# Kernel optimization log

Measured on AMD Instinct MI355X. Metric: run time of the kernel, lower is better.

Reference implementation:

```python
import jax, jax.numpy as jnp
import numpy as np

OUT = 7        # RoIPool output_size
STRIDE = 16    # feature map stride (forward does cat_rois[:,1:] *= 1/16)


def setup_inputs() -> dict:
    key = jax.random.key(0)
    k1, k2, k3 = jax.random.split(key, 3)
    B, C, H, W, N = 2, 256, 50, 50, 128
    features = jax.random.normal(k1, (B, C, H, W), jnp.float32)
    im = jax.random.randint(k2, (N,), 0, B).astype(jnp.float32)
    # image-space coords in [0, 16*(H-1)] so rounded feature coords stay in-bounds
    coords = jax.random.uniform(k3, (N, 4), jnp.float32, 0.0, float(STRIDE * (H - 1)))
    x1 = jnp.minimum(coords[:, 0], coords[:, 2])
    x2 = jnp.maximum(coords[:, 0], coords[:, 2])
    y1 = jnp.minimum(coords[:, 1], coords[:, 3])
    y2 = jnp.maximum(coords[:, 1], coords[:, 3])
    cat_rois = jnp.stack([im, x1, y1, x2, y2], axis=1)
    return {"features": features, "cat_rois": cat_rois}


def _roi_pool(features, cat_rois):
    # cat_rois[:,1:] *= 1/16 ; round ; cast to int (as in the torch module)
    rois = cat_rois.at[:, 1:].multiply(1.0 / STRIDE)
    rois = jnp.round(rois).astype(jnp.int32)
    im = rois[:, 0]
    x1, y1, x2, y2 = rois[:, 1], rois[:, 2], rois[:, 3], rois[:, 4]
    h = y2 - y1 + 1  # slice y1:y2+1 -> height
    w = x2 - x1 + 1
    H, W = features.shape[2], features.shape[3]

    i = jnp.arange(OUT)
    # AdaptiveMaxPool2d bin boundaries: start=floor(i*h/OUT), end=ceil((i+1)*h/OUT)
    ys = (i[None, :] * h[:, None]) // OUT + y1[:, None]                 # [N,OUT]
    ye = ((i[None, :] + 1) * h[:, None] + OUT - 1) // OUT + y1[:, None]
    xs = (i[None, :] * w[:, None]) // OUT + x1[:, None]
    xe = ((i[None, :] + 1) * w[:, None] + OUT - 1) // OUT + x1[:, None]

    r = jnp.arange(H)
    c = jnp.arange(W)
    row_mask = (r[None, None, :] >= ys[:, :, None]) & (r[None, None, :] < ye[:, :, None])  # [N,OUT,H]
    col_mask = (c[None, None, :] >= xs[:, :, None]) & (c[None, None, :] < xe[:, :, None])  # [N,OUT,W]

    feat = features[im]  # gather per-roi image: [N,C,H,W]
    neg = jnp.finfo(features.dtype).min
    # row pooling: small fixed loop over OUT bins; select fuses into reduce-max
    rp = jnp.stack(
        [jnp.max(jnp.where(row_mask[:, i, :][:, None, :, None], feat, neg), axis=2)
         for i in range(OUT)], axis=2)  # [N,C,OUT,W]
    out = jnp.stack(
        [jnp.max(jnp.where(col_mask[:, j, :][:, None, None, :], rp, neg), axis=3)
         for j in range(OUT)], axis=3)  # [N,C,OUT,OUT]
    return out


def reference(features, cat_rois):
    return _roi_pool(features, cat_rois)
```

## Files before the change

### kernel.cpp

```cpp
#include <hip/hip_runtime.h>
#include <float.h>

#define OUTP 7
#define NCH 256
#define FH 50
#define FW 50
#define LDS_W 65

__global__ __launch_bounds__(256) void roi_pool_v5(
    const float* __restrict__ features,
    const float* __restrict__ cat_rois,
    float* __restrict__ out)
{
    __shared__ float rowmax[4][OUTP][LDS_W];

    const int lane = threadIdx.x & 63;
    const int quad = threadIdx.x >> 6;
    const int n    = blockIdx.x >> 6;
    const int c    = ((blockIdx.x & 63) << 2) + quad;

    const float* r5 = cat_rois + n * 5;
    const int im = __builtin_amdgcn_readfirstlane((int)rintf(r5[0]));
    const int x1 = __builtin_amdgcn_readfirstlane((int)rintf(r5[1] * 0.0625f));
    const int y1 = __builtin_amdgcn_readfirstlane((int)rintf(r5[2] * 0.0625f));
    const int x2 = __builtin_amdgcn_readfirstlane((int)rintf(r5[3] * 0.0625f));
    const int y2 = __builtin_amdgcn_readfirstlane((int)rintf(r5[4] * 0.0625f));

    const int h = y2 - y1 + 1;
    const int w = x2 - x1 + 1;

    const float* base = features + ((size_t)(im * NCH + c)) * (FH * FW)
                                 + y1 * FW + x1;

    float rm[OUTP];
    #pragma unroll
    for (int i = 0; i < OUTP; ++i) rm[i] = -FLT_MAX;

    if (lane < w) {
        if (h <= 21) {
            #pragma unroll
            for (int i = 0; i < OUTP; ++i) {
                const int ys  = i * h / OUTP;
                const int ye1 = ((i + 1) * h + OUTP - 1) / OUTP - 1;
                float v0 = base[ys * FW + lane];
                float v1 = base[min(ys + 1, ye1) * FW + lane];
                float v2 = base[min(ys + 2, ye1) * FW + lane];
                float v3 = base[min(ys + 3, ye1) * FW + lane];
                rm[i] = fmaxf(fmaxf(v0, v1), fmaxf(v2, v3));
            }
        } else {
            #pragma unroll
            for (int i = 0; i < OUTP; ++i) {
                const int ys  = i * h / OUTP;
                const int ye1 = ((i + 1) * h + OUTP - 1) / OUTP - 1;
                float v[8];
                #pragma unroll
                for (int k = 0; k < 8; ++k)
                    v[k] = base[min(ys + k, ye1) * FW + lane];
                float m01 = fmaxf(v[0], v[1]), m23 = fmaxf(v[2], v[3]);
                float m45 = fmaxf(v[4], v[5]), m67 = fmaxf(v[6], v[7]);
                rm[i] = fmaxf(fmaxf(m01, m23), fmaxf(m45, m67));
            }
        }
    }

    #pragma unroll
    for (int i = 0; i < OUTP; ++i)
        rowmax[quad][i][lane] = rm[i];

    __syncthreads();

    if (lane < OUTP * OUTP) {
        const int i  = lane / OUTP;
        const int j  = lane % OUTP;
        const int xs = j * w / OUTP;
        const int xe = ((j + 1) * w + OUTP - 1) / OUTP;

        float m = -FLT_MAX;
        for (int x = xs; x < xe; ++x)
            m = fmaxf(m, rowmax[quad][i][x]);

        out[(((size_t)n * NCH + c) * OUTP + i) * OUTP + j] = m;
    }
}

extern "C" void kernel_launch(void* const* d_in, const int* in_sizes, int n_in,
                              void* d_out, int out_size, void* d_ws, size_t ws_size,
                              hipStream_t stream) {
    const float* features = (const float*)d_in[0];
    const float* cat_rois = (const float*)d_in[1];
    float* out = (float*)d_out;

    const int N = in_sizes[1] / 5;
    dim3 grid(N * (NCH / 4));
    roi_pool_v5<<<grid, 256, 0, stream>>>(features, cat_rois, out);
}
```

Measured before the change: 73.61 us.

## Pack multiple channels per wavefront for narrow ROIs and shrink grid

Each wavefront now handles several channels at once when the ROI width is small, splitting its 64 lanes into 16- or 32-lane sub-groups by ROI width. Each block covers 16 channels through multiple passes instead of 4, so the grid is four times smaller. The aim is to stop wasting idle lanes on narrow ROIs and to cut block launch overhead. In exchange, wide ROIs need several serial passes with extra block barriers, and the column-reduce step loops over the packed channels.

```diff
diff --git a/kernel.cpp b/kernel.cpp
--- a/kernel.cpp
+++ b/kernel.cpp
@@ -5,19 +5,19 @@
 #define NCH 256
 #define FH 50
 #define FW 50
-#define LDS_W 65
+#define CHW (FH * FW)
 
-__global__ __launch_bounds__(256) void roi_pool_v5(
+__global__ __launch_bounds__(256) void roi_pool_v6(
     const float* __restrict__ features,
     const float* __restrict__ cat_rois,
     float* __restrict__ out)
 {
-    __shared__ float rowmax[4][OUTP][LDS_W];
+    __shared__ float rowmax[4][OUTP][66];
 
     const int lane = threadIdx.x & 63;
     const int quad = threadIdx.x >> 6;
-    const int n    = blockIdx.x >> 6;
-    const int c    = ((blockIdx.x & 63) << 2) + quad;
+    const int n    = blockIdx.x >> 4;
+    const int c0   = ((blockIdx.x & 15) << 4) + (quad << 2);
 
     const float* r5 = cat_rois + n * 5;
     const int im = __builtin_amdgcn_readfirstlane((int)rintf(r5[0]));
@@ -29,58 +29,72 @@
     const int h = y2 - y1 + 1;
     const int w = x2 - x1 + 1;
 
-    const float* base = features + ((size_t)(im * NCH + c)) * (FH * FW)
-                                 + y1 * FW + x1;
+    const int lwshift = (w <= 16) ? 4 : (w <= 32) ? 5 : 6;
+    const int LW      = 1 << lwshift;
+    const int CP      = 64 >> lwshift;
+    const int npass   = 4 >> (6 - lwshift);
+    const int ch_sub  = lane >> lwshift;
+    const int col     = lane & (LW - 1);
 
-    float rm[OUTP];
-    #pragma unroll
-    for (int i = 0; i < OUTP; ++i) rm[i] = -FLT_MAX;
+    const size_t im_base = (size_t)(im * NCH) * CHW + y1 * FW + x1;
 
-    if (lane < w) {
-        if (h <= 21) {
-            #pragma unroll
-            for (int i = 0; i < OUTP; ++i) {
-                const int ys  = i * h / OUTP;
-                const int ye1 = ((i + 1) * h + OUTP - 1) / OUTP - 1;
-                float v0 = base[ys * FW + lane];
-                float v1 = base[min(ys + 1, ye1) * FW + lane];
-                float v2 = base[min(ys + 2, ye1) * FW + lane];
-                float v3 = base[min(ys + 3, ye1) * FW + lane];
-                rm[i] = fmaxf(fmaxf(v0, v1), fmaxf(v2, v3));
-            }
-        } else {
-            #pragma unroll
-            for (int i = 0; i < OUTP; ++i) {
-                const int ys  = i * h / OUTP;
-                const int ye1 = ((i + 1) * h + OUTP - 1) / OUTP - 1;
-                float v[8];
+    for (int pass = 0; pass < npass; ++pass) {
+        const int cc = c0 + pass * CP + ch_sub;
+        const float* base = features + im_base + (size_t)cc * CHW;
+
+        float rm[OUTP];
+        #pragma unroll
+        for (int i = 0; i < OUTP; ++i) rm[i] = -FLT_MAX;
+
+        if (col < w) {
+            if (h <= 21) {
                 #pragma unroll
-                for (int k = 0; k < 8; ++k)
-                    v[k] = base[min(ys + k, ye1) * FW + lane];
-                float m01 = fmaxf(v[0], v[1]), m23 = fmaxf(v[2], v[3]);
-                float m45 = fmaxf(v[4], v[5]), m67 = fmaxf(v[6], v[7]);
-                rm[i] = fmaxf(fmaxf(m01, m23), fmaxf(m45, m67));
+                for (int i = 0; i < OUTP; ++i) {
+                    const int ys  = i * h / OUTP;
+                    const int ye1 = ((i + 1) * h + OUTP - 1) / OUTP - 1;
+                    float v0 = base[ys * FW + col];
+                    float v1 = base[min(ys + 1, ye1) * FW + col];
+                    float v2 = base[min(ys + 2, ye1) * FW + col];
+                    float v3 = base[min(ys + 3, ye1) * FW + col];
+                    rm[i] = fmaxf(fmaxf(v0, v1), fmaxf(v2, v3));
+                }
+            } else {
+                #pragma unroll
+                for (int i = 0; i < OUTP; ++i) {
+                    const int ys  = i * h / OUTP;
+                    const int ye1 = ((i + 1) * h + OUTP - 1) / OUTP - 1;
+                    float v[8];
+                    #pragma unroll
+                    for (int k = 0; k < 8; ++k)
+                        v[k] = base[min(ys + k, ye1) * FW + col];
+                    rm[i] = fmaxf(fmaxf(fmaxf(v[0], v[1]), fmaxf(v[2], v[3])),
+                                  fmaxf(fmaxf(v[4], v[5]), fmaxf(v[6], v[7])));
+                }
             }
         }
-    }
 
-    #pragma unroll
-    for (int i = 0; i < OUTP; ++i)
-        rowmax[quad][i][lane] = rm[i];
+        #pragma unroll
+        for (int i = 0; i < OUTP; ++i)
+            rowmax[quad][i][lane] = rm[i];
 
-    __syncthreads();
+        __syncthreads();
 
-    if (lane < OUTP * OUTP) {
-        const int i  = lane / OUTP;
-        const int j  = lane % OUTP;
-        const int xs = j * w / OUTP;
-        const int xe = ((j + 1) * w + OUTP - 1) / OUTP;
+        if (lane < OUTP * OUTP) {
+            const int i  = lane / OUTP;
+            const int j  = lane - i * OUTP;
+            const int xs = j * w / OUTP;
+            const int xe = ((j + 1) * w + OUTP - 1) / OUTP;
+            for (int cs = 0; cs < CP; ++cs) {
+                const float* rp = &rowmax[quad][i][cs << lwshift];
+                float m = -FLT_MAX;
+                for (int x = xs; x < xe; ++x)
+                    m = fmaxf(m, rp[x]);
+                out[((size_t)n * NCH + (c0 + pass * CP + cs)) * (OUTP * OUTP)
+                    + lane] = m;
+            }
+        }
 
-        float m = -FLT_MAX;
-        for (int x = xs; x < xe; ++x)
-            m = fmaxf(m, rowmax[quad][i][x]);
-
-        out[(((size_t)n * NCH + c) * OUTP + i) * OUTP + j] = m;
+        __syncthreads();
     }
 }
 
@@ -92,6 +106,6 @@
     float* out = (float*)d_out;
 
     const int N = in_sizes[1] / 5;
-    dim3 grid(N * (NCH / 4));
-    roi_pool_v5<<<grid, 256, 0, stream>>>(features, cat_rois, out);
+    dim3 grid(N * (NCH / 16));
+    roi_pool_v6<<<grid, 256, 0, stream>>>(features, cat_rois, out);
 }
```

New measurement: 74.42 us. Within noise of the previous version (+1.1%).

## Pack columns as float2 across lanes and reduce rows with warp shuffles

Applied to the files above, without the earlier changes.

Row pooling now gives each lane a float2 column pair and spreads the rows of each bin across lane groups. The per-bin row maxima are combined with xor shuffles, not serial loads per lane, and the column loop becomes a fixed 8-tap clamped max. The block-wide __syncthreads is replaced by a block fence, on the basis that each wavefront reads only its own LDS slice. The aim is better lane utilisation when boxes are narrow and fewer loads per lane. In exchange it adds shuffle traffic and relies on bins spanning at most 8 rows per lane group and 8 columns.

```diff
diff --git a/kernel.cpp b/kernel.cpp
--- a/kernel.cpp
+++ b/kernel.cpp
@@ -5,14 +5,18 @@
 #define NCH 256
 #define FH 50
 #define FW 50
-#define LDS_W 65
+#define CHW (FH * FW)
 
-__global__ __launch_bounds__(256) void roi_pool_v5(
+__device__ __forceinline__ float shfl_xor_f(float v, int mask) {
+    return __shfl_xor(v, mask, 64);
+}
+
+__global__ __launch_bounds__(256) void roi_pool_v7(
     const float* __restrict__ features,
     const float* __restrict__ cat_rois,
     float* __restrict__ out)
 {
-    __shared__ float rowmax[4][OUTP][LDS_W];
+    __shared__ float rowmax[4][OUTP][66];
 
     const int lane = threadIdx.x & 63;
     const int quad = threadIdx.x >> 6;
@@ -26,61 +30,76 @@
     const int x2 = __builtin_amdgcn_readfirstlane((int)rintf(r5[3] * 0.0625f));
     const int y2 = __builtin_amdgcn_readfirstlane((int)rintf(r5[4] * 0.0625f));
 
-    const int h = y2 - y1 + 1;
-    const int w = x2 - x1 + 1;
+    const int h   = y2 - y1 + 1;
+    const int w   = x2 - x1 + 1;
+    const int cs2 = x1 >> 1;
+    const int nck = (x2 >> 1) - cs2 + 1;
 
-    const float* base = features + ((size_t)(im * NCH + c)) * (FH * FW)
-                                 + y1 * FW + x1;
+    const int shift = (nck <= 8) ? 3 : (nck <= 16) ? 4 : 5;
+    const int wp    = 1 << shift;
+    const int rpt   = 64 >> shift;
+    const int c4    = lane & (wp - 1);
+    const int rsub  = lane >> shift;
 
-    float rm[OUTP];
+    const int ck = cs2 + min(c4, nck - 1);
+    const float* base = features + (size_t)(im * NCH + c) * CHW + ck * 2;
+
     #pragma unroll
-    for (int i = 0; i < OUTP; ++i) rm[i] = -FLT_MAX;
+    for (int i = 0; i < OUTP; ++i) {
+        const int ys  = i * h / OUTP;
+        const int bh1 = ((i + 1) * h + OUTP - 1) / OUTP - 1 - ys;
 
-    if (lane < w) {
-        if (h <= 21) {
-            #pragma unroll
-            for (int i = 0; i < OUTP; ++i) {
-                const int ys  = i * h / OUTP;
-                const int ye1 = ((i + 1) * h + OUTP - 1) / OUTP - 1;
-                float v0 = base[ys * FW + lane];
-                float v1 = base[min(ys + 1, ye1) * FW + lane];
-                float v2 = base[min(ys + 2, ye1) * FW + lane];
-                float v3 = base[min(ys + 3, ye1) * FW + lane];
-                rm[i] = fmaxf(fmaxf(v0, v1), fmaxf(v2, v3));
+        float mx, my;
+        {
+            const int rr = y1 + ys + min(rsub, bh1);
+            const float2 v = *(const float2*)(base + rr * FW);
+            mx = v.x; my = v.y;
+        }
+        if (shift >= 4) {
+            const int rr = y1 + ys + min(rsub + rpt, bh1);
+            const float2 v = *(const float2*)(base + rr * FW);
+            mx = fmaxf(mx, v.x); my = fmaxf(my, v.y);
+            if (shift == 5) {
+                const int ra = y1 + ys + min(rsub + 2 * rpt, bh1);
+                const int rb = y1 + ys + min(rsub + 3 * rpt, bh1);
+                const float2 va = *(const float2*)(base + ra * FW);
+                const float2 vb = *(const float2*)(base + rb * FW);
+                mx = fmaxf(mx, fmaxf(va.x, vb.x));
+                my = fmaxf(my, fmaxf(va.y, vb.y));
             }
-        } else {
-            #pragma unroll
-            for (int i = 0; i < OUTP; ++i) {
-                const int ys  = i * h / OUTP;
-                const int ye1 = ((i + 1) * h + OUTP - 1) / OUTP - 1;
-                float v[8];
-                #pragma unroll
-                for (int k = 0; k < 8; ++k)
-                    v[k] = base[min(ys + k, ye1) * FW + lane];
-                float m01 = fmaxf(v[0], v[1]), m23 = fmaxf(v[2], v[3]);
-                float m45 = fmaxf(v[4], v[5]), m67 = fmaxf(v[6], v[7]);
-                rm[i] = fmaxf(fmaxf(m01, m23), fmaxf(m45, m67));
-            }
+        }
+
+        mx = fmaxf(mx, shfl_xor_f(mx, 32));
+        my = fmaxf(my, shfl_xor_f(my, 32));
+        if (shift <= 4) {
+            mx = fmaxf(mx, shfl_xor_f(mx, 16));
+            my = fmaxf(my, shfl_xor_f(my, 16));
+        }
+        if (shift <= 3) {
+            mx = fmaxf(mx, shfl_xor_f(mx, 8));
+            my = fmaxf(my, shfl_xor_f(my, 8));
+        }
+
+        if (lane < wp) {
+            rowmax[quad][i][2 * c4]     = mx;
+            rowmax[quad][i][2 * c4 + 1] = my;
         }
     }
 
-    #pragma unroll
-    for (int i = 0; i < OUTP; ++i)
-        rowmax[quad][i][lane] = rm[i];
-
-    __syncthreads();
+    __threadfence_block();
 
     if (lane < OUTP * OUTP) {
-        const int i  = lane / OUTP;
-        const int j  = lane % OUTP;
-        const int xs = j * w / OUTP;
-        const int xe = ((j + 1) * w + OUTP - 1) / OUTP;
-
-        float m = -FLT_MAX;
-        for (int x = xs; x < xe; ++x)
-            m = fmaxf(m, rowmax[quad][i][x]);
-
-        out[(((size_t)n * NCH + c) * OUTP + i) * OUTP + j] = m;
+        const int i   = lane / OUTP;
+        const int j   = lane - i * OUTP;
+        const int d   = x1 & 1;
+        const int xs  = j * w / OUTP + d;
+        const int xe1 = ((j + 1) * w + OUTP - 1) / OUTP - 1 + d;
+        const float* rp = rowmax[quad][i];
+        float m = rp[xs];
+        #pragma unroll
+        for (int k = 1; k < 8; ++k)
+            m = fmaxf(m, rp[min(xs + k, xe1)]);
+        out[((size_t)n * NCH + c) * (OUTP * OUTP) + lane] = m;
     }
 }
 
@@ -93,5 +112,5 @@
 
     const int N = in_sizes[1] / 5;
     dim3 grid(N * (NCH / 4));
-    roi_pool_v5<<<grid, 256, 0, stream>>>(features, cat_rois, out);
+    roi_pool_v7<<<grid, 256, 0, stream>>>(features, cat_rois, out);
 }
```

Result: slower. 77.09 us (+4.7%).
